# Optimization experiments

Hardware: AMD Instinct MI355X
Metric: run time of the kernel (lower is better)

## Reference

```python
import jax, jax.numpy as jnp
import numpy as np
from jax.scipy.special import logsumexp

B, T, V, E, H, K = 64, 512, 21128, 256, 512, 31


def setup_inputs() -> dict:
    key = jax.random.key(0)
    ks = jax.random.split(key, 32)
    s = 1.0 / np.sqrt(H)

    def u(k, shape):
        return jax.random.uniform(k, shape, jnp.float32, -s, s)

    inp = {
        "input_ids": jax.random.randint(ks[0], (B, T), 0, V),
        "labels": jax.random.randint(ks[1], (B, T), 0, K),
        "emb": jax.random.normal(ks[2], (V, E), jnp.float32) * 0.05,
    }
    i = 3
    for layer, insz in (("l0", E), ("l1", 2 * H)):
        for d in ("f", "b"):
            inp["w_ih_%s%s" % (layer, d)] = u(ks[i], (3 * H, insz)); i += 1
            inp["w_hh_%s%s" % (layer, d)] = u(ks[i], (3 * H, H)); i += 1
            inp["b_ih_%s%s" % (layer, d)] = u(ks[i], (3 * H,)); i += 1
            inp["b_hh_%s%s" % (layer, d)] = u(ks[i], (3 * H,)); i += 1
    inp["cls_w"] = u(ks[i], (K, 2 * H))
    inp["cls_b"] = u(ks[i + 1], (K,))
    inp["crf_start"] = jax.random.normal(ks[i + 2], (K,), jnp.float32) * 0.1
    inp["crf_end"] = jax.random.normal(ks[i + 3], (K,), jnp.float32) * 0.1
    inp["crf_trans"] = jax.random.normal(ks[i + 4], (K, K), jnp.float32) * 0.1
    return inp


def gru_dir(x, w_ih, w_hh, b_ih, b_hh, reverse):
    # x: [B, T, in]. PyTorch GRU gate math, gates ordered (r, z, n).
    xp = jnp.einsum('bti,gi->btg', x, w_ih) + b_ih  # [B, T, 3H] precomputed input gates
    if reverse:
        xp = xp[:, ::-1]
    h0 = jnp.zeros((x.shape[0], w_hh.shape[1]), x.dtype)

    def step(h, xt):
        gh = h @ w_hh.T + b_hh
        xr, xz, xn = jnp.split(xt, 3, axis=-1)
        hr, hz, hn = jnp.split(gh, 3, axis=-1)
        r = jax.nn.sigmoid(xr + hr)
        z = jax.nn.sigmoid(xz + hz)
        n = jnp.tanh(xn + r * hn)
        h_new = (1.0 - z) * n + z * h
        return h_new, h_new

    _, hs = jax.lax.scan(step, h0, jnp.swapaxes(xp, 0, 1))
    hs = jnp.swapaxes(hs, 0, 1)  # [B, T, H]
    if reverse:
        hs = hs[:, ::-1]
    return hs


def crf_llh(emissions, tags, mask, start, end, trans):
    # Linear-chain CRF log-likelihood, summed over batch. mask[:, 0] assumed True.
    Bn = emissions.shape[0]
    mf = mask.astype(emissions.dtype)
    bidx = jnp.arange(Bn)
    em_t = jnp.take_along_axis(emissions, tags[:, :, None], axis=2)[:, :, 0]  # [B, T]
    num = start[tags[:, 0]] + em_t[:, 0]
    tr = trans[tags[:, :-1], tags[:, 1:]]  # [B, T-1]
    num = num + jnp.sum((tr + em_t[:, 1:]) * mf[:, 1:], axis=1)
    last_idx = jnp.sum(mask.astype(jnp.int32), axis=1) - 1
    num = num + end[tags[bidx, last_idx]]

    alpha0 = start[None, :] + emissions[:, 0]  # [B, K]

    def step(alpha, inp):
        em, m = inp  # em [B, K], m [B]
        nxt = logsumexp(alpha[:, :, None] + trans[None] + em[:, None, :], axis=1)
        return jnp.where(m[:, None], nxt, alpha), None

    alpha, _ = jax.lax.scan(
        step, alpha0,
        (jnp.swapaxes(emissions[:, 1:], 0, 1), jnp.swapaxes(mask[:, 1:], 0, 1)))
    denom = logsumexp(alpha + end[None, :], axis=1)
    return jnp.sum(num - denom)


def reference(input_ids, labels, emb,
              w_ih_l0f, w_hh_l0f, b_ih_l0f, b_hh_l0f,
              w_ih_l0b, w_hh_l0b, b_ih_l0b, b_hh_l0b,
              w_ih_l1f, w_hh_l1f, b_ih_l1f, b_hh_l1f,
              w_ih_l1b, w_hh_l1b, b_ih_l1b, b_hh_l1b,
              cls_w, cls_b, crf_start, crf_end, crf_trans):
    x = emb[input_ids]  # [B, T, E]
    f0 = gru_dir(x, w_ih_l0f, w_hh_l0f, b_ih_l0f, b_hh_l0f, False)
    b0 = gru_dir(x, w_ih_l0b, w_hh_l0b, b_ih_l0b, b_hh_l0b, True)
    h1 = jnp.concatenate([f0, b0], axis=-1)  # [B, T, 2H]
    f1 = gru_dir(h1, w_ih_l1f, w_hh_l1f, b_ih_l1f, b_hh_l1f, False)
    b1 = gru_dir(h1, w_ih_l1b, w_hh_l1b, b_ih_l1b, b_hh_l1b, True)
    gru_out = jnp.concatenate([f1, b1], axis=-1)  # [B, T, 2H]
    emissions = jnp.einsum('bth,kh->btk', gru_out, cls_w) + cls_b  # [B, T, K]
    mask = labels > -1  # labels.gt(labels_padding_value=-1)
    loss = -crf_llh(emissions, labels, mask, crf_start, crf_end, crf_trans)
    return (loss, emissions)
```

## Files before the change

### kernel.cpp

```cpp
#include <hip/hip_runtime.h>

#define DI __device__ __forceinline__

constexpr int B_  = 64;
constexpr int T_  = 512;
constexpr int E_  = 256;
constexpr int H_  = 512;
constexpr int G_  = 1536;
constexpr int H2_ = 1024;
constexpr int K_  = 31;
constexpr int BT_ = B_ * T_;
constexpr int TC_ = 64;
constexpr int NC_ = T_ / TC_;

typedef float        f32x4  __attribute__((ext_vector_type(4)));
typedef short        bf16x8 __attribute__((ext_vector_type(8)));
typedef unsigned int u32x4  __attribute__((ext_vector_type(4)));
typedef unsigned long long ull;

DI float bf2f(unsigned short u) {
    union { unsigned int i; float f; } v; v.i = ((unsigned int)u) << 16; return v.f;
}
DI unsigned short f2bf(float f) {
    union { float f; unsigned int i; } v; v.f = f;
    unsigned int r = v.i + 0x7fffu + ((v.i >> 16) & 1u);
    return (unsigned short)(r >> 16);
}
DI float sigm(float x) { return 1.f / (1.f + __expf(-x)); }
DI float tanh_(float x) {
    x = fminf(15.f, fmaxf(-15.f, x));
    float e = __expf(-2.f * x);
    return (1.f - e) / (1.f + e);
}

#define MFMA16(a, b, c) __builtin_amdgcn_mfma_f32_16x16x32_bf16(a, b, c, 0, 0, 0)

__global__ void cvt_f32_bf16(const float* __restrict__ src, unsigned short* __restrict__ dst, int n) {
    int i = blockIdx.x * blockDim.x + threadIdx.x;
    int stride = gridDim.x * blockDim.x;
    for (; i < n; i += stride) dst[i] = f2bf(src[i]);
}

__global__ __launch_bounds__(256) void cvt_cls(const float* __restrict__ src,
                                               unsigned short* __restrict__ dstf,
                                               unsigned short* __restrict__ dstb) {
    int i = blockIdx.x * 256 + threadIdx.x;
    if (i >= 32 * H_) return;
    int n = i >> 9, k = i & 511;
    float vf = (n < K_) ? src[n * H2_ + k] : 0.f;
    float vb = (n < K_) ? src[n * H2_ + H_ + k] : 0.f;
    dstf[i] = f2bf(vf);
    dstb[i] = f2bf(vb);
}

__global__ __launch_bounds__(256) void emis_bias_init(const float* __restrict__ cls_b,
                                                      float* __restrict__ out1) {
    int i = blockIdx.x * 256 + threadIdx.x;
    int stride = gridDim.x * 256;
    for (; i < BT_ * K_; i += stride) {
        int n = i - (i / K_) * K_;
        out1[i] = cls_b[n];
    }
}

template <bool OUTF32, bool ACCUM, bool AGATHER>
DI void gemm_tile(unsigned short (*As)[40], unsigned short (*Ws)[40],
                  const unsigned short* A, const float* gsrc, const int* ids, int lda,
                  size_t arow0, const unsigned short* W, int ldw, int nrows, int n0,
                  const float* bias, void* Cout, int ldc, size_t crow0,
                  int nout, int ksz, int tid) {
    const int w = tid >> 6, l = tid & 63;
    const int srow = tid >> 2, sc8 = (tid & 3) * 8;
    const int mw = (w >> 1) * 32, nw = (w & 1) * 32;
    const int fl = l & 15, fk = (l >> 4) * 8;
    f32x4 z4 = { 0.f, 0.f, 0.f, 0.f };
    f32x4 acc[2][2];
    acc[0][0] = z4; acc[0][1] = z4; acc[1][0] = z4; acc[1][1] = z4;
    size_t abase;
    if (AGATHER) abase = (size_t)ids[arow0 + srow] * lda;
    else         abase = (arow0 + srow) * (size_t)lda;

    for (int kc = 0; kc < ksz; kc += 32) {
        u32x4 av, wvv;
        if (AGATHER) {
            const float4* ap = (const float4*)(gsrc + abase + kc + sc8);
            float4 a0 = ap[0], a1 = ap[1];
            union { unsigned short s[8]; u32x4 v; } r;
            r.s[0] = f2bf(a0.x); r.s[1] = f2bf(a0.y); r.s[2] = f2bf(a0.z); r.s[3] = f2bf(a0.w);
            r.s[4] = f2bf(a1.x); r.s[5] = f2bf(a1.y); r.s[6] = f2bf(a1.z); r.s[7] = f2bf(a1.w);
            av = r.v;
        } else {
            av = *(const u32x4*)(A + abase + kc + sc8);
        }
        if (n0 + srow < nrows)
            wvv = *(const u32x4*)(W + (size_t)(n0 + srow) * ldw + kc + sc8);
        else { u32x4 zz = { 0u, 0u, 0u, 0u }; wvv = zz; }
        __syncthreads();
        *(u32x4*)&As[srow][sc8] = av;
        *(u32x4*)&Ws[srow][sc8] = wvv;
        __syncthreads();
        bf16x8 a0 = *(const bf16x8*)&As[mw + fl][fk];
        bf16x8 a1 = *(const bf16x8*)&As[mw + 16 + fl][fk];
        bf16x8 b0 = *(const bf16x8*)&Ws[nw + fl][fk];
        bf16x8 b1 = *(const bf16x8*)&Ws[nw + 16 + fl][fk];
        acc[0][0] = MFMA16(a0, b0, acc[0][0]);
        acc[0][1] = MFMA16(a0, b1, acc[0][1]);
        acc[1][0] = MFMA16(a1, b0, acc[1][0]);
        acc[1][1] = MFMA16(a1, b1, acc[1][1]);
    }

    #pragma unroll
    for (int mf = 0; mf < 2; ++mf)
        #pragma unroll
        for (int nf = 0; nf < 2; ++nf) {
            int col = n0 + nw + nf * 16 + fl;
            if (col >= nout) continue;
            float bv = bias ? bias[col] : 0.f;
            #pragma unroll
            for (int j = 0; j < 4; ++j) {
                int r = mw + mf * 16 + (l >> 4) * 4 + j;
                size_t crow = crow0 + r;
                float v = acc[mf][nf][j] + bv;
                if (OUTF32) {
                    float* C = (float*)Cout;
                    if (ACCUM) C[crow * ldc + col] += v;
                    else       C[crow * ldc + col] = v;
                } else {
                    ((unsigned short*)Cout)[crow * ldc + col] = f2bf(v);
                }
            }
        }
}

template <bool OUTF32, bool ACCUM, bool AGATHER>
__global__ __launch_bounds__(256) void gemm_k(
        const unsigned short* __restrict__ A, const float* __restrict__ gsrc,
        const int* __restrict__ ids, int lda, int m_base, int astride,
        const unsigned short* __restrict__ W, int ldw, int nrows,
        const float* __restrict__ bias,
        void* __restrict__ Cout, int ldc, int c_base, int cstride, int nout, int ksz) {
    __shared__ unsigned short As[64][40];
    __shared__ unsigned short Ws[64][40];
    gemm_tile<OUTF32, ACCUM, AGATHER>(As, Ws, A, gsrc, ids, lda,
        (size_t)m_base + (size_t)blockIdx.x * astride, W, ldw, nrows,
        blockIdx.y * 64, bias, Cout, ldc,
        (size_t)c_base + (size_t)blockIdx.x * cstride, nout, ksz, threadIdx.x);
}

__global__ __launch_bounds__(256) void emis_k(
        const unsigned short* __restrict__ gof, const unsigned short* __restrict__ gob,
        const unsigned short* __restrict__ clsf, const unsigned short* __restrict__ clsb,
        float* __restrict__ out1, int t0f, int t0b) {
    __shared__ unsigned short As[64][40];
    __shared__ unsigned short Ws[64][40];
    const unsigned short* A = blockIdx.y ? gob : gof;
    const unsigned short* W = blockIdx.y ? clsb : clsf;
    int t0 = blockIdx.y ? t0b : t0f;
    gemm_tile<true, true, false>(As, Ws, A, nullptr, nullptr, H_,
        (size_t)blockIdx.x * TC_, W, H_, 32, 0, nullptr,
        (void*)out1, K_, (size_t)t0 + (size_t)blockIdx.x * T_, K_, H_, threadIdx.x);
}

template <bool AGATHER>
__global__ __launch_bounds__(256, 1) void fused_scan_gemm(
        int c, int layer,
        const unsigned short* __restrict__ xpc_f, const unsigned short* __restrict__ xpc_b,
        const unsigned short* __restrict__ whh_f, const unsigned short* __restrict__ whh_b,
        const float* __restrict__ bhh_f, const float* __restrict__ bhh_b,
        unsigned int* __restrict__ hpub,
        float* __restrict__ hcar,
        unsigned short* __restrict__ out_f, unsigned short* __restrict__ out_b,
        int ldo, int mode, int* __restrict__ flags,
        const unsigned short* __restrict__ gA, const float* __restrict__ gsrc,
        const int* __restrict__ gids, int glda,
        const unsigned short* __restrict__ gwf, const unsigned short* __restrict__ gwb,
        const float* __restrict__ gbf, const float* __restrict__ gbb,
        unsigned short* __restrict__ xpf_nxt, unsigned short* __restrict__ xpb_nxt,
        int t0f_n, int t0b_n, int do_gemm) {
    __shared__ __align__(16) char smem[32768];
    const int bid = blockIdx.x;
    const int tid = threadIdx.x;

    if (bid >= 64) {
        if (!do_gemm) return;
        const int gb = bid - 64;
        if (AGATHER) {
            unsigned short (*As)[40] = (unsigned short (*)[40])smem;
            unsigned short (*Ws)[40] = (unsigned short (*)[40])(smem + 5120);
            for (int job = gb; job < 2 * 64 * 24; job += 192) {
                int dirj = job & 1;
                int rest = job >> 1;
                int mt = rest & 63;
                int nt = rest >> 6;
                const unsigned short* gw = dirj ? gwb : gwf;
                const float* gbias = dirj ? gbb : gbf;
                unsigned short* gout = dirj ? xpb_nxt : xpf_nxt;
                int t0 = dirj ? t0b_n : t0f_n;
                gemm_tile<false, false, true>(As, Ws, gA, gsrc, gids, glda,
                    (size_t)t0 + (size_t)mt * T_, gw, glda, G_, nt * 64, gbias,
                    (void*)gout, G_, (size_t)mt * TC_, G_, glda, tid);
            }
        } else {
            unsigned short (*A1)[40] = (unsigned short (*)[40])smem;
            unsigned short (*W1)[40] = (unsigned short (*)[40])(smem + 10240);
            const int w = tid >> 6, l = tid & 63;
            const int fl = l & 15, fk = (l >> 4) * 8;
            const int mw2 = (w >> 1) * 64, nw2 = (w & 1) * 64;
            const int rA = tid >> 1, ch = (tid & 1) * 16;
            #pragma unroll 1
            for (int it = 0; it < 4; ++it) {
                int job = it * 192 + gb;
                int dirj = (job >= 384) ? 1 : 0;
                int jj = job - dirj * 384;
                int nt = jj >> 5;
                int mt2 = jj & 31;
                const unsigned short* gw = dirj ? gwb : gwf;
                const float* gbias = dirj ? gbb : gbf;
                unsigned short* gout = dirj ? xpb_nxt : xpf_nxt;
                int t0 = dirj ? t0b_n : t0f_n;
                int n0j = nt * 128;
                const int mA = mt2 * 2 + (rA >> 6), tlA = rA & 63;
                const unsigned short* aRow = gA + ((size_t)mA * T_ + t0 + tlA) * H2_ + ch;
                const unsigned short* wRow = gw + (size_t)(n0j + rA) * H2_ + ch;
                f32x4 z4 = { 0.f, 0.f, 0.f, 0.f };
                f32x4 acc[4][4];
                #pragma unroll
                for (int a2 = 0; a2 < 4; ++a2)
                    #pragma unroll
                    for (int b2 = 0; b2 < 4; ++b2) acc[a2][b2] = z4;

                for (int kc = 0; kc < H2_; kc += 32) {
                    u32x4 av0 = *(const u32x4*)(aRow + kc);
                    u32x4 av1 = *(const u32x4*)(aRow + kc + 8);
                    u32x4 wv0 = *(const u32x4*)(wRow + kc);
                    u32x4 wv1 = *(const u32x4*)(wRow + kc + 8);
                    __syncthreads();
                    *(u32x4*)&A1[rA][ch] = av0;
                    *(u32x4*)&A1[rA][ch + 8] = av1;
                    *(u32x4*)&W1[rA][ch] = wv0;
                    *(u32x4*)&W1[rA][ch + 8] = wv1;
                    __syncthreads();
                    bf16x8 af[4], bf[4];
                    #pragma unroll
                    for (int a2 = 0; a2 < 4; ++a2) af[a2] = *(const bf16x8*)&A1[mw2 + a2 * 16 + fl][fk];
                    #pragma unroll
                    for (int b2 = 0; b2 < 4; ++b2) bf[b2] = *(const bf16x8*)&W1[nw2 + b2 * 16 + fl][fk];
                    #pragma unroll
                    for (int a2 = 0; a2 < 4; ++a2)
                        #pragma unroll
                        for (int b2 = 0; b2 < 4; ++b2)
                            acc[a2][b2] = MFMA16(af[a2], bf[b2], acc[a2][b2]);
                }

                #pragma unroll
                for (int a2 = 0; a2 < 4; ++a2)
                    #pragma unroll
                    for (int b2 = 0; b2 < 4; ++b2) {
                        int col = n0j + nw2 + b2 * 16 + fl;
                        float bv = gbias[col];
                        #pragma unroll
                        for (int j = 0; j < 4; ++j) {
                            int rloc = mw2 + a2 * 16 + (l >> 4) * 4 + j;
                            int m = mt2 * 2 + (rloc >> 6), tl = rloc & 63;
                            gout[((size_t)m * TC_ + tl) * G_ + col] = f2bf(acc[a2][b2][j] + bv);
                        }
                    }
            }
        }
        return;
    }

    const int dir = bid >> 5;
    const int rb  = bid & 31;
    const int ug  = rb >> 2;
    const int bg  = rb & 3;
    const int w = tid >> 6, l = tid & 63;
    const int fl = l & 15, q = l >> 4, fko = q * 8;
    const unsigned short* xp = dir ? xpc_b : xpc_f;
    const unsigned short* whh = dir ? whh_b : whh_f;
    const float* bhh = dir ? bhh_b : bhh_f;
    unsigned short* outp = dir ? out_b : out_f;
    int* pollb  = flags + (dir * 4 + bg) * 32 * 32;
    int* myflag = pollb + (ug * 4 + w) * 32;

    const int u0w = ug * 64 + w * 16;
    bf16x8 wv[3][16];
    #pragma unroll
    for (int g = 0; g < 3; ++g)
        #pragma unroll
        for (int ks = 0; ks < 16; ++ks)
            wv[g][ks] = *(const bf16x8*)(whh + (size_t)(g * H_ + u0w + fl) * H_ + ks * 32 + fko);

    const int u = u0w + fl;
    const float br_ = bhh[u], bz_ = bhh[H_ + u], bn_ = bhh[2 * H_ + u];
    const int mb = bg * 16 + q * 4;
    const int srowl = tid >> 4;
    const int sseg  = tid & 15;

    float hp[4];
    if (c > 0) {
        #pragma unroll
        for (int j = 0; j < 4; ++j) hp[j] = hcar[dir * (B_ * H_) + (mb + j) * H_ + u];
    } else {
        #pragma unroll
        for (int j = 0; j < 4; ++j) hp[j] = 0.f;
    }

    unsigned short xg[3][4];
    auto ldxp = [&](int tl) {
        #pragma unroll
        for (int j = 0; j < 4; ++j) {
            const unsigned short* xb = xp + ((size_t)((mb + j) * TC_ + tl) * G_) + u;
            xg[0][j] = xb[0]; xg[1][j] = xb[H_]; xg[2][j] = xb[2 * H_];
        }
    };
    ldxp(dir ? (TC_ - 1) : 0);

    for (int sl = 0; sl < TC_; ++sl) {
        const int s  = c * TC_ + sl;
        const int gs = layer * T_ + s;
        const int t = dir ? (T_ - 1 - s) : s;
        const int tloc = dir ? (TC_ - 1 - sl) : sl;

        f32x4 z4 = { 0.f, 0.f, 0.f, 0.f };
        f32x4 acc[3];
        acc[0] = z4; acc[1] = z4; acc[2] = z4;

        if (s > 0) {
            const unsigned int rpar = (unsigned int)(((s - 1) & 1) * 16384);
            if (sl > 0) {
                int v = gs;
                if (l < 32) v = __hip_atomic_load(pollb + l * 32, __ATOMIC_RELAXED, __HIP_MEMORY_SCOPE_AGENT);
                while (!__all(v >= gs)) {
                    __builtin_amdgcn_s_sleep(1);
                    if (l < 32) v = __hip_atomic_load(pollb + l * 32, __ATOMIC_RELAXED, __HIP_MEMORY_SCOPE_AGENT);
                }
                asm volatile("" ::: "memory");
            }
            {
                const ull* src = (const ull*)(hpub
                    + ((size_t)((((s - 1) & 1) * 2 + dir) * B_ + bg * 16 + srowl)) * 256)
                    + sseg * 8;
                ull qv[8];
                #pragma unroll
                for (int i = 0; i < 8; ++i)
                    qv[i] = __hip_atomic_load(src + i, __ATOMIC_RELAXED, __HIP_MEMORY_SCOPE_AGENT);
                char* dst = smem + rpar + srowl * 1024;
                #pragma unroll
                for (int i = 0; i < 4; ++i) {
                    unsigned int byt = (unsigned int)(sseg * 64 + i * 16);
                    byt ^= ((unsigned int)(srowl & 7)) << 4;
                    union { ull qq[2]; u32x4 v4; } pk;
                    pk.qq[0] = qv[2 * i]; pk.qq[1] = qv[2 * i + 1];
                    *(u32x4*)(dst + byt) = pk.v4;
                }
            }
            __syncthreads();
            #pragma unroll
            for (int ks = 0; ks < 16; ++ks) {
                unsigned int byt = (unsigned int)(ks * 64 + q * 16);
                byt ^= ((unsigned int)(fl & 7)) << 4;
                bf16x8 afr = *(const bf16x8*)(smem + rpar + fl * 1024 + byt);
                acc[0] = MFMA16(afr, wv[0][ks], acc[0]);
                acc[1] = MFMA16(afr, wv[1][ks], acc[1]);
                acc[2] = MFMA16(afr, wv[2][ks], acc[2]);
            }
        }

        unsigned short hb16s[4];
        #pragma unroll
        for (int j = 0; j < 4; ++j) {
            float xr = bf2f(xg[0][j]);
            float xz = bf2f(xg[1][j]);
            float xn = bf2f(xg[2][j]);
            float r = sigm(xr + acc[0][j] + br_);
            float z = sigm(xz + acc[1][j] + bz_);
            float nn = tanh_(xn + r * (acc[2][j] + bn_));
            float hv = (1.f - z) * nn + z * hp[j];
            hp[j] = hv;
            hb16s[j] = f2bf(hv);
        }

        unsigned int* hw = hpub + (size_t)((s & 1) * 2 + dir) * (B_ * 256);
        #pragma unroll
        for (int j = 0; j < 4; ++j) {
            unsigned int pv = (unsigned int)(unsigned short)__shfl_xor((int)hb16s[j], 1);
            if ((fl & 1) == 0) {
                unsigned int pk32 = (unsigned int)hb16s[j] | (pv << 16);
                __hip_atomic_store(hw + (size_t)(mb + j) * 256 + (u >> 1), pk32,
                                   __ATOMIC_RELAXED, __HIP_MEMORY_SCOPE_AGENT);
            }
        }
        asm volatile("" ::: "memory");
        #pragma unroll
        for (int j = 0; j < 4; ++j) {
            size_t row = mode ? (size_t)((mb + j) * TC_ + tloc) : ((size_t)(mb + j) * T_ + t);
            outp[row * ldo + u] = hb16s[j];
        }
        if (sl < TC_ - 1) ldxp(dir ? (TC_ - 2 - sl) : (sl + 1));
        asm volatile("s_waitcnt vmcnt(16)" ::: "memory");
        if (l == 0)
            __hip_atomic_store(myflag, gs + 1, __ATOMIC_RELAXED, __HIP_MEMORY_SCOPE_AGENT);
    }

    #pragma unroll
    for (int j = 0; j < 4; ++j) hcar[dir * (B_ * H_) + (mb + j) * H_ + u] = hp[j];
}

__global__ __launch_bounds__(64) void crf_kernel(const float* __restrict__ em,
                                                 const int* __restrict__ labels,
                                                 const float* __restrict__ start,
                                                 const float* __restrict__ endv,
                                                 const float* __restrict__ trans,
                                                 float* __restrict__ partials) {
    __shared__ float tr[32 * 32];
    const int b = blockIdx.x, l = threadIdx.x;
    for (int e2 = l; e2 < 961; e2 += 64) {
        int r = e2 / 31, cc = e2 - r * 31;
        tr[r * 32 + cc] = trans[e2];
    }
    if (l < 32) tr[31 * 32 + l] = 0.f;
    __syncthreads();
    const int* lab = labels + b * T_;
    const float* eb = em + (size_t)b * T_ * K_;

    float part = 0.f, cnt = 0.f;
    for (int t = l; t < T_; t += 64) {
        int lt = lab[t];
        if (lt > -1) {
            cnt += 1.f;
            if (t > 0) part += tr[lab[t - 1] * 32 + lt] + eb[t * K_ + lt];
        }
    }
    #pragma unroll
    for (int o = 32; o; o >>= 1) { part += __shfl_xor(part, o); cnt += __shfl_xor(cnt, o); }
    int lastidx = (int)cnt - 1;
    float num = part + start[lab[0]] + eb[lab[0]] + endv[lab[lastidx]];

    const int jj = l & 31, half = l >> 5;
    const int i0 = half * 16;
    const int ecol = (jj < K_) ? jj : (K_ - 1);
    float a = (jj < K_) ? (start[jj] + eb[jj]) : -3.0e38f;
    for (int t = 1; t < T_; ++t) {
        float tv[16];
        float m = -3.0e38f;
        #pragma unroll
        for (int k = 0; k < 16; ++k) {
            float av = __shfl(a, i0 + k);
            float x = av + tr[(i0 + k) * 32 + jj];
            tv[k] = x;
            m = fmaxf(m, x);
        }
        float ss = 0.f;
        #pragma unroll
        for (int k = 0; k < 16; ++k) ss += __expf(tv[k] - m);
        float m2 = __shfl_xor(m, 32), s2 = __shfl_xor(ss, 32);
        float M = fmaxf(m, m2);
        float S = ss * __expf(m - M) + s2 * __expf(m2 - M);
        float anew = eb[t * K_ + ecol] + M + __logf(S);
        a = ((lab[t] > -1) && (jj < K_)) ? anew : a;
    }
    float v = (jj < K_) ? (a + endv[jj]) : -3.0e38f;
    float m = v;
    #pragma unroll
    for (int o = 32; o; o >>= 1) m = fmaxf(m, __shfl_xor(m, o));
    float ss = (half == 0 && jj < K_) ? __expf(v - m) : 0.f;
    #pragma unroll
    for (int o = 32; o; o >>= 1) ss += __shfl_xor(ss, o);
    if (l == 0) partials[b] = num - (m + __logf(ss));
}

__global__ __launch_bounds__(64) void loss_reduce(const float* __restrict__ partials,
                                                  float* __restrict__ out) {
    float v = partials[threadIdx.x];
    #pragma unroll
    for (int o = 32; o; o >>= 1) v += __shfl_xor(v, o);
    if (threadIdx.x == 0) out[0] = -v;
}

__global__ void sentinel(float* __restrict__ out, float v) { out[0] = -v; }

extern "C" void kernel_launch(void* const* d_in, const int* in_sizes, int n_in,
                              void* d_out, int out_size, void* d_ws, size_t ws_size,
                              hipStream_t stream) {
    const int*   ids      = (const int*)d_in[0];
    const int*   labels   = (const int*)d_in[1];
    const float* emb      = (const float*)d_in[2];
    const float* wih[4]   = { (const float*)d_in[3], (const float*)d_in[7], (const float*)d_in[11], (const float*)d_in[15] };
    const float* whh[4]   = { (const float*)d_in[4], (const float*)d_in[8], (const float*)d_in[12], (const float*)d_in[16] };
    const float* bih[4]   = { (const float*)d_in[5], (const float*)d_in[9], (const float*)d_in[13], (const float*)d_in[17] };
    const float* bhh[4]   = { (const float*)d_in[6], (const float*)d_in[10], (const float*)d_in[14], (const float*)d_in[18] };
    const float* cls_w    = (const float*)d_in[19];
    const float* cls_b    = (const float*)d_in[20];
    const float* c_start  = (const float*)d_in[21];
    const float* c_end    = (const float*)d_in[22];
    const float* c_trans  = (const float*)d_in[23];
    float* out = (float*)d_out;
    float* out1 = out + 1;

    char* p = (char*)d_ws;
    size_t used = 0;
    auto alloc = [&](size_t bytes) -> char* {
        char* r = p;
        size_t a = (bytes + 255) & ~(size_t)255;
        p += a; used += a;
        return r;
    };
    unsigned short* xpF[2]; unsigned short* xpB[2];
    for (int i = 0; i < 2; ++i) {
        xpF[i] = (unsigned short*)alloc((size_t)B_ * TC_ * G_ * 2);
        xpB[i] = (unsigned short*)alloc((size_t)B_ * TC_ * G_ * 2);
    }
    unsigned short* h1   = (unsigned short*)alloc((size_t)BT_ * H2_ * 2);
    unsigned short* gof  = (unsigned short*)alloc((size_t)B_ * TC_ * H_ * 2);
    unsigned short* gob  = (unsigned short*)alloc((size_t)B_ * TC_ * H_ * 2);
    unsigned short* clsf  = (unsigned short*)alloc((size_t)32 * H_ * 2);
    unsigned short* clshb = (unsigned short*)alloc((size_t)32 * H_ * 2);
    unsigned short* whhbf = (unsigned short*)alloc((size_t)G_ * H_ * 2);
    unsigned short* whhbb = (unsigned short*)alloc((size_t)G_ * H_ * 2);
    unsigned short* wihbf = (unsigned short*)alloc((size_t)G_ * H2_ * 2);
    unsigned short* wihbb = (unsigned short*)alloc((size_t)G_ * H2_ * 2);
    unsigned int*   hpub  = (unsigned int*)alloc((size_t)2 * 2 * B_ * 256 * 4);
    float*          hcar  = (float*)alloc((size_t)2 * B_ * H_ * 4);
    float*          partials = (float*)alloc((size_t)B_ * 4);
    int*            flags = (int*)alloc((size_t)2 * 4 * 32 * 32 * 4);

    if (used > ws_size) {
        sentinel<<<dim3(1), dim3(1), 0, stream>>>(out, (float)(ws_size >> 20));
        return;
    }

    hipMemsetAsync(flags, 0, (size_t)2 * 4 * 32 * 32 * 4, stream);
    cvt_cls<<<dim3((32 * H_ + 255) / 256), dim3(256), 0, stream>>>(cls_w, clsf, clshb);
    emis_bias_init<<<dim3(1024), dim3(256), 0, stream>>>(cls_b, out1);

    for (int layer = 0; layer < 2; ++layer) {
        const float* bf_ = bih[layer * 2 + 0];
        const float* bb_ = bih[layer * 2 + 1];
        const float* bhf = bhh[layer * 2 + 0];
        const float* bhb = bhh[layer * 2 + 1];
        const int lda = layer ? H2_ : E_;

        cvt_f32_bf16<<<dim3(2048), dim3(256), 0, stream>>>(whh[layer * 2 + 0], whhbf, G_ * H_);
        cvt_f32_bf16<<<dim3(2048), dim3(256), 0, stream>>>(whh[layer * 2 + 1], whhbb, G_ * H_);
        cvt_f32_bf16<<<dim3(2048), dim3(256), 0, stream>>>(wih[layer * 2 + 0], wihbf, G_ * lda);
        cvt_f32_bf16<<<dim3(2048), dim3(256), 0, stream>>>(wih[layer * 2 + 1], wihbb, G_ * lda);

        if (layer == 0) {
            gemm_k<false, false, true><<<dim3(64, 24), dim3(256), 0, stream>>>(
                nullptr, emb, ids, E_, 0, T_, wihbf, E_, G_, bf_, (void*)xpF[0], G_, 0, TC_, G_, E_);
            gemm_k<false, false, true><<<dim3(64, 24), dim3(256), 0, stream>>>(
                nullptr, emb, ids, E_, T_ - TC_, T_, wihbb, E_, G_, bb_, (void*)xpB[0], G_, 0, TC_, G_, E_);
        } else {
            gemm_k<false, false, false><<<dim3(64, 24), dim3(256), 0, stream>>>(
                h1, nullptr, nullptr, H2_, 0, T_, wihbf, H2_, G_, bf_, (void*)xpF[0], G_, 0, TC_, G_, H2_);
            gemm_k<false, false, false><<<dim3(64, 24), dim3(256), 0, stream>>>(
                h1, nullptr, nullptr, H2_, T_ - TC_, T_, wihbb, H2_, G_, bb_, (void*)xpB[0], G_, 0, TC_, G_, H2_);
        }

        for (int c = 0; c < NC_; ++c) {
            int dg = (c + 1 < NC_) ? 1 : 0;
            int t0f_n = (c + 1) * TC_;
            int t0b_n = T_ - (c + 2) * TC_;
            if (layer == 0) {
                fused_scan_gemm<true><<<dim3(256), dim3(256), 0, stream>>>(
                    c, 0, xpF[c & 1], xpB[c & 1], whhbf, whhbb, bhf, bhb, hpub, hcar,
                    h1, h1 + H_, H2_, 0, flags,
                    nullptr, emb, ids, E_, wihbf, wihbb, bf_, bb_,
                    xpF[(c + 1) & 1], xpB[(c + 1) & 1], t0f_n, t0b_n, dg);
            } else {
                fused_scan_gemm<false><<<dim3(256), dim3(256), 0, stream>>>(
                    c, 1, xpF[c & 1], xpB[c & 1], whhbf, whhbb, bhf, bhb, hpub, hcar,
                    gof, gob, H_, 1, flags,
                    h1, nullptr, nullptr, H2_, wihbf, wihbb, bf_, bb_,
                    xpF[(c + 1) & 1], xpB[(c + 1) & 1], t0f_n, t0b_n, dg);
                int t0f = c * TC_;
                int t0b = T_ - (c + 1) * TC_;
                emis_k<<<dim3(64, 2), dim3(256), 0, stream>>>(gof, gob, clsf, clshb, out1, t0f, t0b);
            }
        }
    }

    crf_kernel<<<dim3(B_), dim3(64), 0, stream>>>(out1, labels, c_start, c_end, c_trans, partials);
    loss_reduce<<<dim3(1), dim3(64), 0, stream>>>(partials, out);
}
```

Baseline: 4.283 ms.

## Use 512-thread blocks so fewer scan blocks carry the recurrent GRU step

Launches the fused scan+GEMM kernel with 512-thread blocks and 224 blocks instead of 256 threads and 256 blocks. The recurrent scan now runs on 32 blocks (16 per direction) of 8 waves each, with each block covering 128 hidden units. Each GEMM block is split into two independent 256-thread halves, each with its own shared-memory region. The aim is to cut the number of blocks taking part in the per-step cross-block flag synchronisation and to spread the hidden-state copy into LDS over more threads. The spin-wait loop also polls a few times before sleeping, to cut wake-up latency. In exchange, each block needs more registers and LDS, and a block-wide barrier now spans two unrelated GEMM halves.

```diff
diff --git a/kernel.cpp b/kernel.cpp
--- a/kernel.cpp
+++ b/kernel.cpp
@@ -162,7 +162,7 @@
 }
 
 template <bool AGATHER>
-__global__ __launch_bounds__(256, 1) void fused_scan_gemm(
+__global__ __launch_bounds__(512, 1) void fused_scan_gemm(
         int c, int layer,
         const unsigned short* __restrict__ xpc_f, const unsigned short* __restrict__ xpc_b,
         const unsigned short* __restrict__ whh_f, const unsigned short* __restrict__ whh_b,
@@ -177,17 +177,20 @@
         const float* __restrict__ gbf, const float* __restrict__ gbb,
         unsigned short* __restrict__ xpf_nxt, unsigned short* __restrict__ xpb_nxt,
         int t0f_n, int t0b_n, int do_gemm) {
-    __shared__ __align__(16) char smem[32768];
+    __shared__ __align__(16) char smem[40960];
     const int bid = blockIdx.x;
     const int tid = threadIdx.x;
 
-    if (bid >= 64) {
+    if (bid >= 32) {
         if (!do_gemm) return;
-        const int gb = bid - 64;
+        const int qid = (bid - 32) * 2 + (tid >> 8);
+        const int ltid = tid & 255;
+        char* qb = smem + (size_t)(tid >> 8) * 20480;
         if (AGATHER) {
-            unsigned short (*As)[40] = (unsigned short (*)[40])smem;
-            unsigned short (*Ws)[40] = (unsigned short (*)[40])(smem + 5120);
-            for (int job = gb; job < 2 * 64 * 24; job += 192) {
+            unsigned short (*As)[40] = (unsigned short (*)[40])qb;
+            unsigned short (*Ws)[40] = (unsigned short (*)[40])(qb + 5120);
+            #pragma unroll 1
+            for (int job = qid; job < 2 * 64 * 24; job += 384) {
                 int dirj = job & 1;
                 int rest = job >> 1;
                 int mt = rest & 63;
@@ -198,18 +201,18 @@
                 int t0 = dirj ? t0b_n : t0f_n;
                 gemm_tile<false, false, true>(As, Ws, gA, gsrc, gids, glda,
                     (size_t)t0 + (size_t)mt * T_, gw, glda, G_, nt * 64, gbias,
-                    (void*)gout, G_, (size_t)mt * TC_, G_, glda, tid);
+                    (void*)gout, G_, (size_t)mt * TC_, G_, glda, ltid);
             }
         } else {
-            unsigned short (*A1)[40] = (unsigned short (*)[40])smem;
-            unsigned short (*W1)[40] = (unsigned short (*)[40])(smem + 10240);
-            const int w = tid >> 6, l = tid & 63;
+            unsigned short (*A1)[40] = (unsigned short (*)[40])qb;
+            unsigned short (*W1)[40] = (unsigned short (*)[40])(qb + 10240);
+            const int w = ltid >> 6, l = ltid & 63;
             const int fl = l & 15, fk = (l >> 4) * 8;
             const int mw2 = (w >> 1) * 64, nw2 = (w & 1) * 64;
-            const int rA = tid >> 1, ch = (tid & 1) * 16;
+            const int rA = ltid >> 1, ch = (ltid & 1) * 16;
             #pragma unroll 1
-            for (int it = 0; it < 4; ++it) {
-                int job = it * 192 + gb;
+            for (int it = 0; it < 2; ++it) {
+                int job = it * 384 + qid;
                 int dirj = (job >= 384) ? 1 : 0;
                 int jj = job - dirj * 384;
                 int nt = jj >> 5;
@@ -270,10 +273,10 @@
         return;
     }
 
-    const int dir = bid >> 5;
-    const int rb  = bid & 31;
-    const int ug  = rb >> 2;
-    const int bg  = rb & 3;
+    const int dir = bid >> 4;
+    const int rest = bid & 15;
+    const int ug  = rest >> 2;
+    const int bg  = rest & 3;
     const int w = tid >> 6, l = tid & 63;
     const int fl = l & 15, q = l >> 4, fko = q * 8;
     const unsigned short* xp = dir ? xpc_b : xpc_f;
@@ -281,9 +284,9 @@
     const float* bhh = dir ? bhh_b : bhh_f;
     unsigned short* outp = dir ? out_b : out_f;
     int* pollb  = flags + (dir * 4 + bg) * 32 * 32;
-    int* myflag = pollb + (ug * 4 + w) * 32;
-
-    const int u0w = ug * 64 + w * 16;
+    int* myflag = pollb + (ug * 8 + w) * 32;
+
+    const int u0w = ug * 128 + w * 16;
     bf16x8 wv[3][16];
     #pragma unroll
     for (int g = 0; g < 3; ++g)
@@ -294,8 +297,8 @@
     const int u = u0w + fl;
     const float br_ = bhh[u], bz_ = bhh[H_ + u], bn_ = bhh[2 * H_ + u];
     const int mb = bg * 16 + q * 4;
-    const int srowl = tid >> 4;
-    const int sseg  = tid & 15;
+    const int srowl = tid >> 5;
+    const int sseg  = tid & 31;
 
     float hp[4];
     if (c > 0) {
@@ -330,9 +333,10 @@
             const unsigned int rpar = (unsigned int)(((s - 1) & 1) * 16384);
             if (sl > 0) {
                 int v = gs;
+                int tries = 0;
                 if (l < 32) v = __hip_atomic_load(pollb + l * 32, __ATOMIC_RELAXED, __HIP_MEMORY_SCOPE_AGENT);
                 while (!__all(v >= gs)) {
-                    __builtin_amdgcn_s_sleep(1);
+                    if (++tries > 3) __builtin_amdgcn_s_sleep(1);
                     if (l < 32) v = __hip_atomic_load(pollb + l * 32, __ATOMIC_RELAXED, __HIP_MEMORY_SCOPE_AGENT);
                 }
                 asm volatile("" ::: "memory");
@@ -340,15 +344,15 @@
             {
                 const ull* src = (const ull*)(hpub
                     + ((size_t)((((s - 1) & 1) * 2 + dir) * B_ + bg * 16 + srowl)) * 256)
-                    + sseg * 8;
-                ull qv[8];
+                    + sseg * 4;
+                ull qv[4];
                 #pragma unroll
-                for (int i = 0; i < 8; ++i)
+                for (int i = 0; i < 4; ++i)
                     qv[i] = __hip_atomic_load(src + i, __ATOMIC_RELAXED, __HIP_MEMORY_SCOPE_AGENT);
                 char* dst = smem + rpar + srowl * 1024;
                 #pragma unroll
-                for (int i = 0; i < 4; ++i) {
-                    unsigned int byt = (unsigned int)(sseg * 64 + i * 16);
+                for (int i = 0; i < 2; ++i) {
+                    unsigned int byt = (unsigned int)(sseg * 32 + i * 16);
                     byt ^= ((unsigned int)(srowl & 7)) << 4;
                     union { ull qq[2]; u32x4 v4; } pk;
                     pk.qq[0] = qv[2 * i]; pk.qq[1] = qv[2 * i + 1];
@@ -563,13 +567,13 @@
             int t0f_n = (c + 1) * TC_;
             int t0b_n = T_ - (c + 2) * TC_;
             if (layer == 0) {
-                fused_scan_gemm<true><<<dim3(256), dim3(256), 0, stream>>>(
+                fused_scan_gemm<true><<<dim3(224), dim3(512), 0, stream>>>(
                     c, 0, xpF[c & 1], xpB[c & 1], whhbf, whhbb, bhf, bhb, hpub, hcar,
                     h1, h1 + H_, H2_, 0, flags,
                     nullptr, emb, ids, E_, wihbf, wihbb, bf_, bb_,
                     xpF[(c + 1) & 1], xpB[(c + 1) & 1], t0f_n, t0b_n, dg);
             } else {
-                fused_scan_gemm<false><<<dim3(256), dim3(256), 0, stream>>>(
+                fused_scan_gemm<false><<<dim3(224), dim3(512), 0, stream>>>(
                     c, 1, xpF[c & 1], xpB[c & 1], whhbf, whhbb, bhf, bhb, hpub, hcar,
                     gof, gob, H_, 1, flags,
                     h1, nullptr, nullptr, H2_, wihbf, wihbb, bf_, bb_,
```

Measured after the change: 6.351 ms. +48.3%, slower.

## Fuse emission GEMM for previous chunk into layer-1 scan kernel helper blocks

Applied to the files above, without the earlier changes.

Double-buffers the layer-1 GRU output chunks and has spare helper blocks of the fused scan kernel compute the classifier emissions for the previous chunk, so the separate per-chunk emission launch goes away and its work overlaps the recurrent scan. The last chunk's emissions run in one trailing launch. The spin-wait on peer flags now polls a few times before sleeping, to cut wake-up latency. Costs are extra workspace for the second buffer and more register/shared pressure in the helper blocks.

```diff
diff --git a/kernel.cpp b/kernel.cpp
--- a/kernel.cpp
+++ b/kernel.cpp
@@ -176,15 +176,18 @@
         const unsigned short* __restrict__ gwf, const unsigned short* __restrict__ gwb,
         const float* __restrict__ gbf, const float* __restrict__ gbb,
         unsigned short* __restrict__ xpf_nxt, unsigned short* __restrict__ xpb_nxt,
-        int t0f_n, int t0b_n, int do_gemm) {
+        int t0f_n, int t0b_n, int do_gemm,
+        const unsigned short* __restrict__ egof, const unsigned short* __restrict__ egob,
+        const unsigned short* __restrict__ clsf, const unsigned short* __restrict__ clsb,
+        float* __restrict__ out1, int t0f_e, int t0b_e, int do_emis) {
     __shared__ __align__(16) char smem[32768];
     const int bid = blockIdx.x;
     const int tid = threadIdx.x;
 
     if (bid >= 64) {
-        if (!do_gemm) return;
         const int gb = bid - 64;
         if (AGATHER) {
+            if (!do_gemm) return;
             unsigned short (*As)[40] = (unsigned short (*)[40])smem;
             unsigned short (*Ws)[40] = (unsigned short (*)[40])(smem + 5120);
             for (int job = gb; job < 2 * 64 * 24; job += 192) {
@@ -201,70 +204,82 @@
                     (void*)gout, G_, (size_t)mt * TC_, G_, glda, tid);
             }
         } else {
-            unsigned short (*A1)[40] = (unsigned short (*)[40])smem;
-            unsigned short (*W1)[40] = (unsigned short (*)[40])(smem + 10240);
-            const int w = tid >> 6, l = tid & 63;
-            const int fl = l & 15, fk = (l >> 4) * 8;
-            const int mw2 = (w >> 1) * 64, nw2 = (w & 1) * 64;
-            const int rA = tid >> 1, ch = (tid & 1) * 16;
-            #pragma unroll 1
-            for (int it = 0; it < 4; ++it) {
-                int job = it * 192 + gb;
-                int dirj = (job >= 384) ? 1 : 0;
-                int jj = job - dirj * 384;
-                int nt = jj >> 5;
-                int mt2 = jj & 31;
-                const unsigned short* gw = dirj ? gwb : gwf;
-                const float* gbias = dirj ? gbb : gbf;
-                unsigned short* gout = dirj ? xpb_nxt : xpf_nxt;
-                int t0 = dirj ? t0b_n : t0f_n;
-                int n0j = nt * 128;
-                const int mA = mt2 * 2 + (rA >> 6), tlA = rA & 63;
-                const unsigned short* aRow = gA + ((size_t)mA * T_ + t0 + tlA) * H2_ + ch;
-                const unsigned short* wRow = gw + (size_t)(n0j + rA) * H2_ + ch;
-                f32x4 z4 = { 0.f, 0.f, 0.f, 0.f };
-                f32x4 acc[4][4];
-                #pragma unroll
-                for (int a2 = 0; a2 < 4; ++a2)
-                    #pragma unroll
-                    for (int b2 = 0; b2 < 4; ++b2) acc[a2][b2] = z4;
-
-                for (int kc = 0; kc < H2_; kc += 32) {
-                    u32x4 av0 = *(const u32x4*)(aRow + kc);
-                    u32x4 av1 = *(const u32x4*)(aRow + kc + 8);
-                    u32x4 wv0 = *(const u32x4*)(wRow + kc);
-                    u32x4 wv1 = *(const u32x4*)(wRow + kc + 8);
-                    __syncthreads();
-                    *(u32x4*)&A1[rA][ch] = av0;
-                    *(u32x4*)&A1[rA][ch + 8] = av1;
-                    *(u32x4*)&W1[rA][ch] = wv0;
-                    *(u32x4*)&W1[rA][ch + 8] = wv1;
-                    __syncthreads();
-                    bf16x8 af[4], bf[4];
-                    #pragma unroll
-                    for (int a2 = 0; a2 < 4; ++a2) af[a2] = *(const bf16x8*)&A1[mw2 + a2 * 16 + fl][fk];
-                    #pragma unroll
-                    for (int b2 = 0; b2 < 4; ++b2) bf[b2] = *(const bf16x8*)&W1[nw2 + b2 * 16 + fl][fk];
+            if (do_gemm) {
+                unsigned short (*A1)[40] = (unsigned short (*)[40])smem;
+                unsigned short (*W1)[40] = (unsigned short (*)[40])(smem + 10240);
+                const int w = tid >> 6, l = tid & 63;
+                const int fl = l & 15, fk = (l >> 4) * 8;
+                const int mw2 = (w >> 1) * 64, nw2 = (w & 1) * 64;
+                const int rA = tid >> 1, ch = (tid & 1) * 16;
+                #pragma unroll 1
+                for (int it = 0; it < 4; ++it) {
+                    int job = it * 192 + gb;
+                    int dirj = (job >= 384) ? 1 : 0;
+                    int jj = job - dirj * 384;
+                    int nt = jj >> 5;
+                    int mt2 = jj & 31;
+                    const unsigned short* gw = dirj ? gwb : gwf;
+                    const float* gbias = dirj ? gbb : gbf;
+                    unsigned short* gout = dirj ? xpb_nxt : xpf_nxt;
+                    int t0 = dirj ? t0b_n : t0f_n;
+                    int n0j = nt * 128;
+                    const int mA = mt2 * 2 + (rA >> 6), tlA = rA & 63;
+                    const unsigned short* aRow = gA + ((size_t)mA * T_ + t0 + tlA) * H2_ + ch;
+                    const unsigned short* wRow = gw + (size_t)(n0j + rA) * H2_ + ch;
+                    f32x4 z4 = { 0.f, 0.f, 0.f, 0.f };
+                    f32x4 acc[4][4];
                     #pragma unroll
                     for (int a2 = 0; a2 < 4; ++a2)
                         #pragma unroll
-                        for (int b2 = 0; b2 < 4; ++b2)
-                            acc[a2][b2] = MFMA16(af[a2], bf[b2], acc[a2][b2]);
+                        for (int b2 = 0; b2 < 4; ++b2) acc[a2][b2] = z4;
+
+                    for (int kc = 0; kc < H2_; kc += 32) {
+                        u32x4 av0 = *(const u32x4*)(aRow + kc);
+                        u32x4 av1 = *(const u32x4*)(aRow + kc + 8);
+                        u32x4 wv0 = *(const u32x4*)(wRow + kc);
+                        u32x4 wv1 = *(const u32x4*)(wRow + kc + 8);
+                        __syncthreads();
+                        *(u32x4*)&A1[rA][ch] = av0;
+                        *(u32x4*)&A1[rA][ch + 8] = av1;
+                        *(u32x4*)&W1[rA][ch] = wv0;
+                        *(u32x4*)&W1[rA][ch + 8] = wv1;
+                        __syncthreads();
+                        bf16x8 af[4], bf[4];
+                        #pragma unroll
+                        for (int a2 = 0; a2 < 4; ++a2) af[a2] = *(const bf16x8*)&A1[mw2 + a2 * 16 + fl][fk];
+                        #pragma unroll
+                        for (int b2 = 0; b2 < 4; ++b2) bf[b2] = *(const bf16x8*)&W1[nw2 + b2 * 16 + fl][fk];
+                        #pragma unroll
+                        for (int a2 = 0; a2 < 4; ++a2)
+                            #pragma unroll
+                            for (int b2 = 0; b2 < 4; ++b2)
+                                acc[a2][b2] = MFMA16(af[a2], bf[b2], acc[a2][b2]);
+                    }
+
+                    #pragma unroll
+                    for (int a2 = 0; a2 < 4; ++a2)
+                        #pragma unroll
+                        for (int b2 = 0; b2 < 4; ++b2) {
+                            int col = n0j + nw2 + b2 * 16 + fl;
+                            float bv = gbias[col];
+                            #pragma unroll
+                            for (int j = 0; j < 4; ++j) {
+                                int rloc = mw2 + a2 * 16 + (l >> 4) * 4 + j;
+                                int m = mt2 * 2 + (rloc >> 6), tl = rloc & 63;
+                                gout[((size_t)m * TC_ + tl) * G_ + col] = f2bf(acc[a2][b2][j] + bv);
+                            }
+                        }
                 }
-
-                #pragma unroll
-                for (int a2 = 0; a2 < 4; ++a2)
-                    #pragma unroll
-                    for (int b2 = 0; b2 < 4; ++b2) {
-                        int col = n0j + nw2 + b2 * 16 + fl;
-                        float bv = gbias[col];
-                        #pragma unroll
-                        for (int j = 0; j < 4; ++j) {
-                            int rloc = mw2 + a2 * 16 + (l >> 4) * 4 + j;
-                            int m = mt2 * 2 + (rloc >> 6), tl = rloc & 63;
-                            gout[((size_t)m * TC_ + tl) * G_ + col] = f2bf(acc[a2][b2][j] + bv);
-                        }
-                    }
+            }
+            if (do_emis && gb < 128) {
+                int dirj = gb >> 6, mt = gb & 63;
+                const unsigned short* A = dirj ? egob : egof;
+                const unsigned short* W = dirj ? clsb : clsf;
+                int t0 = dirj ? t0b_e : t0f_e;
+                gemm_tile<true, true, false>((unsigned short (*)[40])smem,
+                    (unsigned short (*)[40])(smem + 5120),
+                    A, nullptr, nullptr, H_, (size_t)mt * TC_, W, H_, 32, 0, nullptr,
+                    (void*)out1, K_, (size_t)t0 + (size_t)mt * T_, K_, H_, tid);
             }
         }
         return;
@@ -330,9 +345,10 @@
             const unsigned int rpar = (unsigned int)(((s - 1) & 1) * 16384);
             if (sl > 0) {
                 int v = gs;
+                int tries = 0;
                 if (l < 32) v = __hip_atomic_load(pollb + l * 32, __ATOMIC_RELAXED, __HIP_MEMORY_SCOPE_AGENT);
                 while (!__all(v >= gs)) {
-                    __builtin_amdgcn_s_sleep(1);
+                    if (++tries > 3) __builtin_amdgcn_s_sleep(1);
                     if (l < 32) v = __hip_atomic_load(pollb + l * 32, __ATOMIC_RELAXED, __HIP_MEMORY_SCOPE_AGENT);
                 }
                 asm volatile("" ::: "memory");
@@ -512,8 +528,11 @@
         xpB[i] = (unsigned short*)alloc((size_t)B_ * TC_ * G_ * 2);
     }
     unsigned short* h1   = (unsigned short*)alloc((size_t)BT_ * H2_ * 2);
-    unsigned short* gof  = (unsigned short*)alloc((size_t)B_ * TC_ * H_ * 2);
-    unsigned short* gob  = (unsigned short*)alloc((size_t)B_ * TC_ * H_ * 2);
+    unsigned short* goF[2]; unsigned short* goB[2];
+    for (int i = 0; i < 2; ++i) {
+        goF[i] = (unsigned short*)alloc((size_t)B_ * TC_ * H_ * 2);
+        goB[i] = (unsigned short*)alloc((size_t)B_ * TC_ * H_ * 2);
+    }
     unsigned short* clsf  = (unsigned short*)alloc((size_t)32 * H_ * 2);
     unsigned short* clshb = (unsigned short*)alloc((size_t)32 * H_ * 2);
     unsigned short* whhbf = (unsigned short*)alloc((size_t)G_ * H_ * 2);
@@ -567,19 +586,24 @@
                     c, 0, xpF[c & 1], xpB[c & 1], whhbf, whhbb, bhf, bhb, hpub, hcar,
                     h1, h1 + H_, H2_, 0, flags,
                     nullptr, emb, ids, E_, wihbf, wihbb, bf_, bb_,
-                    xpF[(c + 1) & 1], xpB[(c + 1) & 1], t0f_n, t0b_n, dg);
+                    xpF[(c + 1) & 1], xpB[(c + 1) & 1], t0f_n, t0b_n, dg,
+                    nullptr, nullptr, nullptr, nullptr, nullptr, 0, 0, 0);
             } else {
+                int de = (c > 0) ? 1 : 0;
+                int t0f_e = (c - 1) * TC_;
+                int t0b_e = T_ - c * TC_;
                 fused_scan_gemm<false><<<dim3(256), dim3(256), 0, stream>>>(
                     c, 1, xpF[c & 1], xpB[c & 1], whhbf, whhbb, bhf, bhb, hpub, hcar,
-                    gof, gob, H_, 1, flags,
+                    goF[c & 1], goB[c & 1], H_, 1, flags,
                     h1, nullptr, nullptr, H2_, wihbf, wihbb, bf_, bb_,
-                    xpF[(c + 1) & 1], xpB[(c + 1) & 1], t0f_n, t0b_n, dg);
-                int t0f = c * TC_;
-                int t0b = T_ - (c + 1) * TC_;
-                emis_k<<<dim3(64, 2), dim3(256), 0, stream>>>(gof, gob, clsf, clshb, out1, t0f, t0b);
-            }
-        }
-    }
+                    xpF[(c + 1) & 1], xpB[(c + 1) & 1], t0f_n, t0b_n, dg,
+                    goF[(c + 1) & 1], goB[(c + 1) & 1], clsf, clshb, out1, t0f_e, t0b_e, de);
+            }
+        }
+    }
+
+    emis_k<<<dim3(64, 2), dim3(256), 0, stream>>>(goF[(NC_ - 1) & 1], goB[(NC_ - 1) & 1],
+        clsf, clshb, out1, (NC_ - 1) * TC_, 0);
 
     crf_kernel<<<dim3(B_), dim3(64), 0, stream>>>(out1, labels, c_start, c_end, c_trans, partials);
     loss_reduce<<<dim3(1), dim3(64), 0, stream>>>(partials, out);
```

Measured after the change: 4.149 ms. 1.03x faster.
